# Kernel optimization log

Measured on AMD Instinct MI355X. Metric: run time of the kernel, lower is better.

Reference implementation:

```python
import jax, jax.numpy as jnp
import numpy as np

B, S, D, H = 2, 2048, 1024, 16
DH = D // H
EPS = 1e-5


def setup_inputs() -> dict:
    key = jax.random.key(0)
    ks = jax.random.split(key, 12)
    inp = {
        "Q_source": jax.random.normal(ks[0], (B, S, D), jnp.float32),
        "K_source": jax.random.normal(ks[1], (B, S, D), jnp.float32),
        "V_source": jax.random.normal(ks[2], (B, S, D), jnp.float32),
        "padding_mask": jnp.zeros((B, 1, 1, S), dtype=bool),  # no padded keys (avoids NaN rows)
        "future_mask": jnp.triu(jnp.ones((S, S), dtype=bool), k=1)[None, None],  # causal
    }
    sc = 1.0 / np.sqrt(D)
    names = ["WQ", "WK", "WV", "WO"]
    for i, n in enumerate(names):
        inp[n] = jax.random.normal(ks[3 + i], (D, D), jnp.float32) * sc
        inp["b" + n[1]] = jnp.zeros((D,), jnp.float32)
    inp["gamma"] = jnp.ones((D,), jnp.float32)
    inp["beta"] = jnp.zeros((D,), jnp.float32)
    return inp


def reference(Q_source, K_source, V_source, padding_mask, future_mask,
              WQ, bQ, WK, bK, WV, bV, WO, bO, gamma, beta):
    b = Q_source.shape[0]
    # torch Linear: x @ W.T + b ; reshape to [B, H, S, DH]
    def proj(x, W, bb):
        y = x @ W.T + bb
        return y.reshape(b, -1, H, DH).transpose(0, 2, 1, 3)

    Q = proj(Q_source, WQ, bQ)
    K = proj(K_source, WK, bK)
    V = proj(V_source, WV, bV)

    scores = jnp.einsum("bhqd,bhkd->bhqk", Q, K) / jnp.sqrt(jnp.float32(DH))
    neg_inf = jnp.float32(-jnp.inf)
    scores = jnp.where(padding_mask, neg_inf, scores)
    scores = jnp.where(future_mask, neg_inf, scores)
    attn = jax.nn.softmax(scores, axis=-1)

    ctx = jnp.einsum("bhqk,bhkd->bhqd", attn, V)
    ctx = ctx.transpose(0, 2, 1, 3).reshape(b, -1, D)
    out = ctx @ WO.T + bO

    x = Q_source + out
    mu = x.mean(-1, keepdims=True)
    var = x.var(-1, keepdims=True)
    return (x - mu) * jax.lax.rsqrt(var + EPS) * gamma + beta
```

## Files before the change

kernel.cpp:

```cpp
#include <hip/hip_runtime.h>

#define S_LEN 2048
#define DMODEL 1024
#define NH 16
#define DHD 64

typedef __attribute__((ext_vector_type(8))) short bh8;
typedef __attribute__((ext_vector_type(4))) float f32x4;
typedef __attribute__((ext_vector_type(2))) unsigned int u32x2;
typedef __attribute__((ext_vector_type(4))) unsigned int u32x4;
typedef unsigned short u16;
typedef unsigned int u32;

static __device__ __forceinline__ u16 f2bf(float f) {
    unsigned u = __builtin_bit_cast(unsigned, f);
    u += 0x7fffu + ((u >> 16) & 1u);
    return (u16)(u >> 16);
}

typedef const __attribute__((address_space(1))) void* gptr_t;
typedef __attribute__((address_space(3))) void* lptr_t;

static __device__ __forceinline__ void gll16(const void* g, void* l) {
    __builtin_amdgcn_global_load_lds((gptr_t)g, (lptr_t)l, 16, 0, 0);
}

__global__ __launch_bounds__(256) void cvt_all(const float* __restrict__ WQ, const float* __restrict__ WK,
                                               const float* __restrict__ WV, const float* __restrict__ WO,
                                               const float* __restrict__ S0, const float* __restrict__ S1,
                                               const float* __restrict__ S2,
                                               u16* __restrict__ wq, u16* __restrict__ wk,
                                               u16* __restrict__ wv, u16* __restrict__ wo,
                                               u16* __restrict__ q0, u16* __restrict__ k0,
                                               u16* __restrict__ v0) {
    int bid = blockIdx.x;
    const float* s;
    u16* o;
    size_t base;
    if (bid < 2048) {
        int wi = bid >> 9;
        s = wi == 0 ? WQ : (wi == 1 ? WK : (wi == 2 ? WV : WO));
        o = wi == 0 ? wq : (wi == 1 ? wk : (wi == 2 ? wv : wo));
        base = (size_t)(bid & 511) * 2048;
    } else {
        int r = bid - 2048;
        int si = r >> 11;
        s = si == 0 ? S0 : (si == 1 ? S1 : S2);
        o = si == 0 ? q0 : (si == 1 ? k0 : v0);
        base = (size_t)(r & 2047) * 2048;
    }
    size_t i = base + (size_t)threadIdx.x * 8;
    float4 a = *(const float4*)(s + i);
    float4 b = *(const float4*)(s + i + 4);
    u32 p0 = (u32)f2bf(a.x) | ((u32)f2bf(a.y) << 16);
    u32 p1 = (u32)f2bf(a.z) | ((u32)f2bf(a.w) << 16);
    u32 p2 = (u32)f2bf(b.x) | ((u32)f2bf(b.y) << 16);
    u32 p3 = (u32)f2bf(b.z) | ((u32)f2bf(b.w) << 16);
    *(u32x4*)(o + i) = (u32x4){p0, p1, p2, p3};
}

template <int BM, int OBF, int AF32>
static __device__ __forceinline__ void gemm_body(const void* __restrict__ Ap, const u16* __restrict__ Bm,
                                                 const float* __restrict__ bias, void* __restrict__ Cv,
                                                 int N, int K, int bi, int bj, short* Al, short* Bl,
                                                 float oscale) {
    constexpr int MI = BM / 32;
    constexpr int NC = BM / 64;
    int tid = threadIdx.x, lane = tid & 63, w = tid >> 6;
    int ln = lane & 15, hi = lane >> 4;
    int wm = w >> 1, wn = w & 1;
    f32x4 acc[MI][4];
#pragma unroll
    for (int i = 0; i < MI; i++)
#pragma unroll
        for (int j = 0; j < 4; j++) acc[i][j] = (f32x4){0.f, 0.f, 0.f, 0.f};
    int nk = K >> 5;

    float4 fa[NC][2];
    auto loadA = [&](int kt) {
#pragma unroll
        for (int c = 0; c < NC; ++c) {
            int o = c * 4096 + tid * 16;
            int row = o >> 6, e0 = (o & 63) >> 1;
            const float* src = (const float*)Ap + (size_t)(bi * BM + row) * K + kt * 32 + e0;
            fa[c][0] = *(const float4*)src;
            fa[c][1] = *(const float4*)(src + 4);
        }
    };
    auto writeA = [&](int buf) {
#pragma unroll
        for (int c = 0; c < NC; ++c) {
            int o = c * 4096 + tid * 16;
            u32 w0 = (u32)f2bf(fa[c][0].x) | ((u32)f2bf(fa[c][0].y) << 16);
            u32 w1 = (u32)f2bf(fa[c][0].z) | ((u32)f2bf(fa[c][0].w) << 16);
            u32 w2 = (u32)f2bf(fa[c][1].x) | ((u32)f2bf(fa[c][1].y) << 16);
            u32 w3 = (u32)f2bf(fa[c][1].z) | ((u32)f2bf(fa[c][1].w) << 16);
            *(u32x4*)((char*)(Al + buf * (BM * 32)) + o) = (u32x4){w0, w1, w2, w3};
        }
    };
    auto stageA_lds = [&](int buf, int kt) {
#pragma unroll
        for (int c = 0; c < NC; ++c) {
            int o = c * 4096 + tid * 16;
            int row = o >> 6, col = (o & 63) >> 1;
            gll16((const u16*)Ap + (size_t)(bi * BM + row) * K + kt * 32 + col,
                  (char*)(Al + buf * (BM * 32)) + o);
        }
    };
    auto stageB = [&](int buf, int kt) {
#pragma unroll
        for (int c = 0; c < 2; ++c) {
            int o = c * 4096 + tid * 16;
            int row = o >> 6, col = (o & 63) >> 1;
            gll16(Bm + (size_t)(bj * 128 + row) * K + kt * 32 + col, (char*)(Bl + buf * 4096) + o);
        }
    };

    if constexpr (AF32) { loadA(0); writeA(0); } else { stageA_lds(0, 0); }
    stageB(0, 0);
    __syncthreads();
    int cur = 0;
    for (int kt = 0; kt < nk; ++kt) {
        bool pre = (kt + 1 < nk);
        if (pre) {
            if constexpr (AF32) loadA(kt + 1); else stageA_lds(cur ^ 1, kt + 1);
            stageB(cur ^ 1, kt + 1);
        }
        bh8 av[MI], bv[4];
#pragma unroll
        for (int i = 0; i < MI; i++) av[i] = *(const bh8*)&Al[cur * (BM * 32) + (wm * (BM / 2) + i * 16 + ln) * 32 + hi * 8];
#pragma unroll
        for (int j = 0; j < 4; j++) bv[j] = *(const bh8*)&Bl[cur * 4096 + (wn * 64 + j * 16 + ln) * 32 + hi * 8];
#pragma unroll
        for (int i = 0; i < MI; i++)
#pragma unroll
            for (int j = 0; j < 4; j++)
                acc[i][j] = __builtin_amdgcn_mfma_f32_16x16x32_bf16(av[i], bv[j], acc[i][j], 0, 0, 0);
        if constexpr (AF32) { if (pre) writeA(cur ^ 1); }
        __syncthreads();
        cur ^= 1;
    }
    if constexpr (OBF == 2) {
#pragma unroll
        for (int j = 0; j < 4; j++) {
            int col = wn * 64 + j * 16 + ln;
            float bvs = bias[bj * 128 + col];
#pragma unroll
            for (int i = 0; i < MI; i++) {
                int row0 = wm * (BM / 2) + i * 16 + hi * 4;
                u32 p01 = (u32)f2bf(acc[i][j][0] + bvs) | ((u32)f2bf(acc[i][j][1] + bvs) << 16);
                u32 p23 = (u32)f2bf(acc[i][j][2] + bvs) | ((u32)f2bf(acc[i][j][3] + bvs) << 16);
                int idx = col * 128 + (row0 ^ ((col & 7) << 3));
                *(u32x2*)&Al[idx] = (u32x2){p01, p23};
            }
        }
        __syncthreads();
        int b = bi >> 4;
        int sbase = (bi & 15) * 128;
#pragma unroll
        for (int it = 0; it < 8; ++it) {
            int idx = it * 256 + tid;
            int dcol = idx >> 4;
            int sl = (idx & 15) * 8;
            bh8 v = *(const bh8*)&Al[dcol * 128 + (sl ^ ((dcol & 7) << 3))];
            int h = bj * 2 + (dcol >> 6), d = dcol & 63;
            *(bh8*)((u16*)Cv + ((size_t)((b * 16 + h) * 64 + d)) * 2048 + sbase + sl) = v;
        }
        return;
    }
#pragma unroll
    for (int j = 0; j < 4; j++) {
        int col = bj * 128 + wn * 64 + j * 16 + ln;
        float bvs = bias[col];
#pragma unroll
        for (int i = 0; i < MI; i++) {
            int row0 = bi * BM + wm * (BM / 2) + i * 16 + hi * 4;
#pragma unroll
            for (int rr = 0; rr < 4; rr++) {
                if (OBF) {
                    float v = (acc[i][j][rr] + bvs) * oscale;
                    ((u16*)Cv)[(size_t)(row0 + rr) * N + col] = f2bf(v);
                } else {
                    ((float*)Cv)[(size_t)(row0 + rr) * N + col] = acc[i][j][rr] + bvs;
                }
            }
        }
    }
}

__global__ __launch_bounds__(256, 3) void gemm_qkv(const u16* __restrict__ A0, const u16* __restrict__ A1,
                                                   const u16* __restrict__ A2, const u16* __restrict__ B0,
                                                   const u16* __restrict__ B1, const u16* __restrict__ B2,
                                                   const float* __restrict__ c0, const float* __restrict__ c1,
                                                   const float* __restrict__ c2, u16* __restrict__ C0,
                                                   u16* __restrict__ C1, u16* __restrict__ VT) {
    __shared__ short SH[16384];
    short* Al = SH;
    short* Bl = SH + 8192;
    int bid = blockIdx.x;
    int swz = (bid & 7) * 96 + (bid >> 3);
    int z = swz >> 8, t = swz & 255;
    if (z == 2) {
        gemm_body<128, 2, 0>(A2, B2, c2, VT, 1024, 1024, t >> 3, t & 7, Al, Bl, 1.0f);
    } else if (z == 0) {
        gemm_body<128, 1, 0>(A0, B0, c0, C0, 1024, 1024, t >> 3, t & 7, Al, Bl, 0.18033688f);
    } else {
        gemm_body<128, 1, 0>(A1, B1, c1, C1, 1024, 1024, t >> 3, t & 7, Al, Bl, 1.0f);
    }
}

__global__ __launch_bounds__(256) void gemm_o(const u16* __restrict__ A, const u16* __restrict__ Bm,
                                              const float* __restrict__ bias, float* __restrict__ C) {
    __shared__ short Al[2 * 64 * 32];
    __shared__ short Bl[2 * 128 * 32];
    int bid = blockIdx.x;
    int swz = (bid & 7) * 64 + (bid >> 3);
    gemm_body<64, 0, 0>(A, Bm, bias, C, 1024, 1024, swz >> 3, swz & 7, Al, Bl, 1.0f);
}

template <int PLO, int PHI>
static __device__ __forceinline__ void attn_core(const u16* __restrict__ Qp, const u16* __restrict__ Kp,
                                                 const u16* __restrict__ VT, u16* __restrict__ Ctx,
                                                 short* Klb, short* Vlb, short* Pw, float* Csh, float* Ls,
                                                 int b, int h, int bh, int qt, int tid) {
    int lane = tid & 63, w = tid >> 6;
    int grp = w >> 2;
    int qsub = w & 3;
    int tgl = tid & 255;
    int ln = lane & 15, hi = lane >> 4;
    __builtin_amdgcn_s_setprio(PLO);
    bh8 ones;
#pragma unroll
    for (int e = 0; e < 8; e++) ones[e] = (short)0x3F80;

    auto stage_kv = [&](int buf, int kt) {
#pragma unroll
        for (int c = 0; c < 2; ++c) {
            int o = c * 4096 + tgl * 16;
            int rr = o >> 7;
            int slot = (o >> 4) & 7;
            gll16(Kp + ((size_t)(b * S_LEN + kt * 64 + rr)) * DMODEL + h * DHD + ((slot ^ (rr & 7)) << 3),
                  (char*)(Klb + buf * 4096) + o);
            gll16(VT + ((size_t)(bh * DHD + rr)) * S_LEN + kt * 64 + ((slot ^ (rr & 7)) << 3),
                  (char*)(Vlb + buf * 4096) + o);
        }
    };

    int nh = qt + 1;
    int nt = 2 * qt + 2;
    int kbase = grp * nh;
    int qg0 = (qt << 7) + qsub * 32 + ln;
    const bh8* qr0 = (const bh8*)(Qp + ((size_t)(b * S_LEN + qg0)) * DMODEL + h * DHD);
    const bh8* qr1 = (const bh8*)(Qp + ((size_t)(b * S_LEN + qg0 + 16)) * DMODEL + h * DHD);
    bh8 qf[2][2];
    qf[0][0] = qr0[hi]; qf[0][1] = qr0[4 + hi];
    qf[1][0] = qr1[hi]; qf[1][1] = qr1[4 + hi];
    f32x4 ctxa[2][4];
    f32x4 lacc[2];
#pragma unroll
    for (int g = 0; g < 2; g++) {
        lacc[g] = (f32x4){0.f, 0.f, 0.f, 0.f};
#pragma unroll
        for (int i = 0; i < 4; i++) ctxa[g][i] = (f32x4){0.f, 0.f, 0.f, 0.f};
    }
    stage_kv(0, kbase);
    __syncthreads();
    int cur = 0;
    for (int i = 0; i < nh; ++i) {
        int kt = kbase + i;
        if (i + 1 < nh) stage_kv(cur ^ 1, kt + 1);
        f32x4 sc[2][4];
#pragma unroll
        for (int g = 0; g < 2; g++)
#pragma unroll
            for (int ks = 0; ks < 4; ++ks) sc[g][ks] = (f32x4){0.f, 0.f, 0.f, 0.f};
        __builtin_amdgcn_s_setprio(PHI);
#pragma unroll
        for (int dwin = 0; dwin < 2; ++dwin) {
#pragma unroll
            for (int ks = 0; ks < 4; ++ks) {
                int rr = ks * 16 + ln;
                bh8 kv = *(const bh8*)&Klb[cur * 4096 + rr * 64 + ((dwin * 32 + hi * 8) ^ ((rr & 7) << 3))];
                sc[0][ks] = __builtin_amdgcn_mfma_f32_16x16x32_bf16(kv, qf[0][dwin], sc[0][ks], 0, 0, 0);
                sc[1][ks] = __builtin_amdgcn_mfma_f32_16x16x32_bf16(kv, qf[1][dwin], sc[1][ks], 0, 0, 0);
            }
        }
        __builtin_amdgcn_s_setprio(PLO);
        if (kt >= nt - 2) {
#pragma unroll
            for (int g = 0; g < 2; g++) {
                int qgq = qg0 + g * 16;
#pragma unroll
                for (int ks = 0; ks < 4; ++ks)
#pragma unroll
                    for (int rr = 0; rr < 4; ++rr) {
                        int kg = kt * 64 + ks * 16 + hi * 4 + rr;
                        sc[g][ks][rr] = (kg <= qgq) ? sc[g][ks][rr] : -1e30f;
                    }
            }
        }
#pragma unroll
        for (int g = 0; g < 2; g++) {
#pragma unroll
            for (int ks = 0; ks < 4; ++ks) {
                u32 u0 = __builtin_bit_cast(u32, __builtin_amdgcn_exp2f(sc[g][ks][0]));
                u32 u1 = __builtin_bit_cast(u32, __builtin_amdgcn_exp2f(sc[g][ks][1]));
                u32 u2 = __builtin_bit_cast(u32, __builtin_amdgcn_exp2f(sc[g][ks][2]));
                u32 u3 = __builtin_bit_cast(u32, __builtin_amdgcn_exp2f(sc[g][ks][3]));
                u32 a01 = (u0 >> 16) | (u1 & 0xffff0000u);
                u32 a23 = (u2 >> 16) | (u3 & 0xffff0000u);
                int kloc = ks * 16 + hi * 4;
                *(u32x2*)&Pw[(g * 16 + ln) * 64 + (kloc ^ ((ln & 7) << 3))] = (u32x2){a01, a23};
            }
        }
        __builtin_amdgcn_s_setprio(PHI);
#pragma unroll
        for (int kw = 0; kw < 2; ++kw) {
            bh8 pf0 = *(const bh8*)&Pw[ln * 64 + ((kw * 32 + hi * 8) ^ ((ln & 7) << 3))];
            bh8 pf1 = *(const bh8*)&Pw[(16 + ln) * 64 + ((kw * 32 + hi * 8) ^ ((ln & 7) << 3))];
            lacc[0] = __builtin_amdgcn_mfma_f32_16x16x32_bf16(ones, pf0, lacc[0], 0, 0, 0);
            lacc[1] = __builtin_amdgcn_mfma_f32_16x16x32_bf16(ones, pf1, lacc[1], 0, 0, 0);
#pragma unroll
            for (int ds = 0; ds < 4; ++ds) {
                int d = ds * 16 + ln;
                bh8 vf = *(const bh8*)&Vlb[cur * 4096 + d * 64 + ((kw * 32 + hi * 8) ^ ((d & 7) << 3))];
                ctxa[0][ds] = __builtin_amdgcn_mfma_f32_16x16x32_bf16(vf, pf0, ctxa[0][ds], 0, 0, 0);
                ctxa[1][ds] = __builtin_amdgcn_mfma_f32_16x16x32_bf16(vf, pf1, ctxa[1][ds], 0, 0, 0);
            }
        }
        __builtin_amdgcn_s_setprio(PLO);
        __syncthreads();
        cur ^= 1;
    }
    __builtin_amdgcn_s_setprio(0);
    if (grp == 1) {
#pragma unroll
        for (int g = 0; g < 2; g++) {
            int qloc = g * 16 + ln;
#pragma unroll
            for (int ds = 0; ds < 4; ++ds) {
                int doff = (ds * 16 + hi * 4) ^ ((qloc & 7) << 3);
                *(f32x4*)&Csh[(qsub * 32 + qloc) * 64 + doff] = ctxa[g][ds];
            }
            if (hi == 0) Ls[qsub * 32 + qloc] = lacc[g][0];
        }
    }
    __syncthreads();
    if (grp == 0) {
#pragma unroll
        for (int g = 0; g < 2; g++) {
            int qloc = g * 16 + ln;
            float inv = 1.f / (lacc[g][0] + Ls[qsub * 32 + qloc]);
            u16* cp = Ctx + ((size_t)(b * S_LEN + qg0 + g * 16)) * DMODEL + h * DHD;
#pragma unroll
            for (int ds = 0; ds < 4; ++ds) {
                int doff = (ds * 16 + hi * 4) ^ ((qloc & 7) << 3);
                f32x4 p = *(const f32x4*)&Csh[(qsub * 32 + qloc) * 64 + doff];
                ushort4 st;
                st.x = f2bf((ctxa[g][ds][0] + p[0]) * inv);
                st.y = f2bf((ctxa[g][ds][1] + p[1]) * inv);
                st.z = f2bf((ctxa[g][ds][2] + p[2]) * inv);
                st.w = f2bf((ctxa[g][ds][3] + p[3]) * inv);
                *(ushort4*)(cp + ds * 16 + hi * 4) = st;
            }
        }
    }
}

__global__ __launch_bounds__(512, 1) void attn_fwd(const u16* __restrict__ Qp, const u16* __restrict__ Kp,
                                                   const u16* __restrict__ VT, u16* __restrict__ Ctx) {
    __shared__ short Kl[2][2][4096];
    __shared__ short Vl[2][2][4096];
    __shared__ short Pl[8][2048];
    __shared__ float Ls[128];
    int tid = threadIdx.x, w = tid >> 6;
    int grp = w >> 2;
    int bid = blockIdx.x;
    int rnd = bid >> 8, slot = bid & 255;
    int xcd = slot & 7, t = slot >> 3;
    int bh = xcd * 4 + (t & 3);
    int qte = t >> 2;
    int qt = rnd ? (15 - 2 * qte) : (2 * qte);
    int b = bh >> 4, h = bh & 15;
    float* Csh = (float*)&Kl[0][0][0];
    if (qt >= 8)
        attn_core<2, 3>(Qp, Kp, VT, Ctx, &Kl[grp][0][0], &Vl[grp][0][0], &Pl[w][0], Csh, Ls, b, h, bh, qt, tid);
    else
        attn_core<0, 1>(Qp, Kp, VT, Ctx, &Kl[grp][0][0], &Vl[grp][0][0], &Pl[w][0], Csh, Ls, b, h, bh, qt, tid);
}

__global__ __launch_bounds__(256) void ln_res(const float* __restrict__ Xres, const float* __restrict__ Y,
                                              const float* __restrict__ gamma, const float* __restrict__ beta,
                                              float* __restrict__ out) {
    int row = blockIdx.x, tid = threadIdx.x;
    const float4* xr = (const float4*)(Xres + (size_t)row * DMODEL);
    const float4* yr = (const float4*)(Y + (size_t)row * DMODEL);
    float4 a = xr[tid], bq = yr[tid];
    float x0 = a.x + bq.x, x1 = a.y + bq.y, x2 = a.z + bq.z, x3 = a.w + bq.w;
    float s1 = x0 + x1 + x2 + x3;
    float s2 = x0 * x0 + x1 * x1 + x2 * x2 + x3 * x3;
#pragma unroll
    for (int off = 32; off > 0; off >>= 1) {
        s1 += __shfl_xor(s1, off);
        s2 += __shfl_xor(s2, off);
    }
    __shared__ float r1[4], r2[4];
    int wv = tid >> 6;
    if ((tid & 63) == 0) { r1[wv] = s1; r2[wv] = s2; }
    __syncthreads();
    s1 = r1[0] + r1[1] + r1[2] + r1[3];
    s2 = r2[0] + r2[1] + r2[2] + r2[3];
    float mu = s1 * (1.0f / 1024.0f);
    float var = s2 * (1.0f / 1024.0f) - mu * mu;
    float rstd = rsqrtf(var + 1e-5f);
    const float4* g4 = (const float4*)gamma;
    const float4* b4 = (const float4*)beta;
    float4 g = g4[tid], bb = b4[tid];
    float4 res;
    res.x = (x0 - mu) * rstd * g.x + bb.x;
    res.y = (x1 - mu) * rstd * g.y + bb.y;
    res.z = (x2 - mu) * rstd * g.z + bb.z;
    res.w = (x3 - mu) * rstd * g.w + bb.w;
    *((float4*)(out + (size_t)row * DMODEL) + tid) = res;
}

extern "C" void kernel_launch(void* const* d_in, const int* in_sizes, int n_in,
                              void* d_out, int out_size, void* d_ws, size_t ws_size,
                              hipStream_t stream) {
    const float* Qs = (const float*)d_in[0];
    const float* Ks = (const float*)d_in[1];
    const float* Vs = (const float*)d_in[2];
    const float* WQ = (const float*)d_in[5];
    const float* bQ = (const float*)d_in[6];
    const float* WK = (const float*)d_in[7];
    const float* bK = (const float*)d_in[8];
    const float* WV = (const float*)d_in[9];
    const float* bV = (const float*)d_in[10];
    const float* WO = (const float*)d_in[11];
    const float* bO = (const float*)d_in[12];
    const float* gamma = (const float*)d_in[13];
    const float* beta = (const float*)d_in[14];

    const size_t MB = 1u << 20;
    char* w8 = (char*)d_ws;
    u16* Qb  = (u16*)(w8 + 0 * MB);
    u16* Kb  = (u16*)(w8 + 8 * MB);
    u16* Vb  = (u16*)(w8 + 16 * MB);
    u16* WQb = (u16*)(w8 + 24 * MB);
    u16* WKb = (u16*)(w8 + 26 * MB);
    u16* WVb = (u16*)(w8 + 28 * MB);
    u16* WOb = (u16*)(w8 + 30 * MB);
    u16* Qp  = (u16*)(w8 + 32 * MB);
    u16* Kp  = (u16*)(w8 + 40 * MB);
    u16* VTb = (u16*)(w8 + 56 * MB);
    u16* Ctx = (u16*)(w8 + 64 * MB);
    float* Y2 = (float*)(w8 + 72 * MB);

    cvt_all<<<8192, 256, 0, stream>>>(WQ, WK, WV, WO, Qs, Ks, Vs, WQb, WKb, WVb, WOb, Qb, Kb, Vb);
    gemm_qkv<<<768, 256, 0, stream>>>(Qb, Kb, Vb, WQb, WKb, WVb, bQ, bK, bV, Qp, Kp, VTb);
    attn_fwd<<<512, 512, 0, stream>>>(Qp, Kp, VTb, Ctx);
    gemm_o<<<512, 256, 0, stream>>>(Ctx, WOb, bO, Y2);
    ln_res<<<4096, 256, 0, stream>>>(Qs, Y2, gamma, beta, (float*)d_out);
}
```

Before: 112.9 us.

## Replace MFMA rowsum with scalar sums, halve P scratch, raise attention occupancy

The softmax denominator is now accumulated as fp32 scalar sums with cross-lane shuffles, replacing the extra MFMA against a vector of ones. The P tile is written and consumed one 16-row group at a time, which halves the per-wave P scratch, and the row-sum buffer now aliases a P buffer. Launch bounds go from 1 to 4 blocks per CU, and the block mapping changes from a zigzag over two rounds to descending query tiles so the longest causal tiles start first. The tighter register budget may cause spills, and processing the groups one after the other adds LDS round trips and reduces MFMA interleaving.

Result: slower. 117.9 us (+4.4%).

```diff
diff --git a/kernel.cpp b/kernel.cpp
--- a/kernel.cpp
+++ b/kernel.cpp
@@ -221,7 +221,7 @@
 template <int PLO, int PHI>
 static __device__ __forceinline__ void attn_core(const u16* __restrict__ Qp, const u16* __restrict__ Kp,
                                                  const u16* __restrict__ VT, u16* __restrict__ Ctx,
-                                                 short* Klb, short* Vlb, short* Pw, float* Csh, float* Ls,
+                                                 short* Klb, short* Vlb, short* Pw, float* Csh, float* Lsh,
                                                  int b, int h, int bh, int qt, int tid) {
     int lane = tid & 63, w = tid >> 6;
     int grp = w >> 2;
@@ -229,9 +229,6 @@
     int tgl = tid & 255;
     int ln = lane & 15, hi = lane >> 4;
     __builtin_amdgcn_s_setprio(PLO);
-    bh8 ones;
-#pragma unroll
-    for (int e = 0; e < 8; e++) ones[e] = (short)0x3F80;
 
     auto stage_kv = [&](int buf, int kt) {
 #pragma unroll
@@ -256,13 +253,11 @@
     qf[0][0] = qr0[hi]; qf[0][1] = qr0[4 + hi];
     qf[1][0] = qr1[hi]; qf[1][1] = qr1[4 + hi];
     f32x4 ctxa[2][4];
-    f32x4 lacc[2];
-#pragma unroll
-    for (int g = 0; g < 2; g++) {
-        lacc[g] = (f32x4){0.f, 0.f, 0.f, 0.f};
+    float ls[2] = {0.f, 0.f};
+#pragma unroll
+    for (int g = 0; g < 2; g++)
 #pragma unroll
         for (int i = 0; i < 4; i++) ctxa[g][i] = (f32x4){0.f, 0.f, 0.f, 0.f};
-    }
     stage_kv(0, kbase);
     __syncthreads();
     int cur = 0;
@@ -303,34 +298,40 @@
         for (int g = 0; g < 2; g++) {
 #pragma unroll
             for (int ks = 0; ks < 4; ++ks) {
-                u32 u0 = __builtin_bit_cast(u32, __builtin_amdgcn_exp2f(sc[g][ks][0]));
-                u32 u1 = __builtin_bit_cast(u32, __builtin_amdgcn_exp2f(sc[g][ks][1]));
-                u32 u2 = __builtin_bit_cast(u32, __builtin_amdgcn_exp2f(sc[g][ks][2]));
-                u32 u3 = __builtin_bit_cast(u32, __builtin_amdgcn_exp2f(sc[g][ks][3]));
+                float p0 = __builtin_amdgcn_exp2f(sc[g][ks][0]);
+                float p1 = __builtin_amdgcn_exp2f(sc[g][ks][1]);
+                float p2 = __builtin_amdgcn_exp2f(sc[g][ks][2]);
+                float p3 = __builtin_amdgcn_exp2f(sc[g][ks][3]);
+                ls[g] += (p0 + p1) + (p2 + p3);
+                u32 u0 = __builtin_bit_cast(u32, p0);
+                u32 u1 = __builtin_bit_cast(u32, p1);
+                u32 u2 = __builtin_bit_cast(u32, p2);
+                u32 u3 = __builtin_bit_cast(u32, p3);
                 u32 a01 = (u0 >> 16) | (u1 & 0xffff0000u);
                 u32 a23 = (u2 >> 16) | (u3 & 0xffff0000u);
                 int kloc = ks * 16 + hi * 4;
-                *(u32x2*)&Pw[(g * 16 + ln) * 64 + (kloc ^ ((ln & 7) << 3))] = (u32x2){a01, a23};
-            }
-        }
-        __builtin_amdgcn_s_setprio(PHI);
-#pragma unroll
-        for (int kw = 0; kw < 2; ++kw) {
-            bh8 pf0 = *(const bh8*)&Pw[ln * 64 + ((kw * 32 + hi * 8) ^ ((ln & 7) << 3))];
-            bh8 pf1 = *(const bh8*)&Pw[(16 + ln) * 64 + ((kw * 32 + hi * 8) ^ ((ln & 7) << 3))];
-            lacc[0] = __builtin_amdgcn_mfma_f32_16x16x32_bf16(ones, pf0, lacc[0], 0, 0, 0);
-            lacc[1] = __builtin_amdgcn_mfma_f32_16x16x32_bf16(ones, pf1, lacc[1], 0, 0, 0);
-#pragma unroll
-            for (int ds = 0; ds < 4; ++ds) {
-                int d = ds * 16 + ln;
-                bh8 vf = *(const bh8*)&Vlb[cur * 4096 + d * 64 + ((kw * 32 + hi * 8) ^ ((d & 7) << 3))];
-                ctxa[0][ds] = __builtin_amdgcn_mfma_f32_16x16x32_bf16(vf, pf0, ctxa[0][ds], 0, 0, 0);
-                ctxa[1][ds] = __builtin_amdgcn_mfma_f32_16x16x32_bf16(vf, pf1, ctxa[1][ds], 0, 0, 0);
-            }
-        }
-        __builtin_amdgcn_s_setprio(PLO);
+                *(u32x2*)&Pw[ln * 64 + (kloc ^ ((ln & 7) << 3))] = (u32x2){a01, a23};
+            }
+            __builtin_amdgcn_s_setprio(PHI);
+#pragma unroll
+            for (int kw = 0; kw < 2; ++kw) {
+                bh8 pf = *(const bh8*)&Pw[ln * 64 + ((kw * 32 + hi * 8) ^ ((ln & 7) << 3))];
+#pragma unroll
+                for (int ds = 0; ds < 4; ++ds) {
+                    int d = ds * 16 + ln;
+                    bh8 vf = *(const bh8*)&Vlb[cur * 4096 + d * 64 + ((kw * 32 + hi * 8) ^ ((d & 7) << 3))];
+                    ctxa[g][ds] = __builtin_amdgcn_mfma_f32_16x16x32_bf16(vf, pf, ctxa[g][ds], 0, 0, 0);
+                }
+            }
+            __builtin_amdgcn_s_setprio(PLO);
+        }
         __syncthreads();
         cur ^= 1;
+    }
+#pragma unroll
+    for (int g = 0; g < 2; g++) {
+        ls[g] += __shfl_xor(ls[g], 16);
+        ls[g] += __shfl_xor(ls[g], 32);
     }
     __builtin_amdgcn_s_setprio(0);
     if (grp == 1) {
@@ -342,7 +343,7 @@
                 int doff = (ds * 16 + hi * 4) ^ ((qloc & 7) << 3);
                 *(f32x4*)&Csh[(qsub * 32 + qloc) * 64 + doff] = ctxa[g][ds];
             }
-            if (hi == 0) Ls[qsub * 32 + qloc] = lacc[g][0];
+            if (hi == 0) Lsh[qsub * 32 + qloc] = ls[g];
         }
     }
     __syncthreads();
@@ -350,7 +351,7 @@
 #pragma unroll
         for (int g = 0; g < 2; g++) {
             int qloc = g * 16 + ln;
-            float inv = 1.f / (lacc[g][0] + Ls[qsub * 32 + qloc]);
+            float inv = 1.f / (ls[g] + Lsh[qsub * 32 + qloc]);
             u16* cp = Ctx + ((size_t)(b * S_LEN + qg0 + g * 16)) * DMODEL + h * DHD;
 #pragma unroll
             for (int ds = 0; ds < 4; ++ds) {
@@ -367,26 +368,24 @@
     }
 }
 
-__global__ __launch_bounds__(512, 1) void attn_fwd(const u16* __restrict__ Qp, const u16* __restrict__ Kp,
+__global__ __launch_bounds__(512, 4) void attn_fwd(const u16* __restrict__ Qp, const u16* __restrict__ Kp,
                                                    const u16* __restrict__ VT, u16* __restrict__ Ctx) {
     __shared__ short Kl[2][2][4096];
     __shared__ short Vl[2][2][4096];
-    __shared__ short Pl[8][2048];
-    __shared__ float Ls[128];
+    __shared__ short Pl[8][1024];
     int tid = threadIdx.x, w = tid >> 6;
     int grp = w >> 2;
     int bid = blockIdx.x;
-    int rnd = bid >> 8, slot = bid & 255;
-    int xcd = slot & 7, t = slot >> 3;
-    int bh = xcd * 4 + (t & 3);
-    int qte = t >> 2;
-    int qt = rnd ? (15 - 2 * qte) : (2 * qte);
+    int xcd = bid & 7;
+    int qt = 15 - (bid >> 5);
+    int bh = xcd * 4 + ((bid >> 3) & 3);
     int b = bh >> 4, h = bh & 15;
     float* Csh = (float*)&Kl[0][0][0];
+    float* Lsh = (float*)&Pl[4][0];
     if (qt >= 8)
-        attn_core<2, 3>(Qp, Kp, VT, Ctx, &Kl[grp][0][0], &Vl[grp][0][0], &Pl[w][0], Csh, Ls, b, h, bh, qt, tid);
+        attn_core<2, 3>(Qp, Kp, VT, Ctx, &Kl[grp][0][0], &Vl[grp][0][0], &Pl[w][0], Csh, Lsh, b, h, bh, qt, tid);
     else
-        attn_core<0, 1>(Qp, Kp, VT, Ctx, &Kl[grp][0][0], &Vl[grp][0][0], &Pl[w][0], Csh, Ls, b, h, bh, qt, tid);
+        attn_core<0, 1>(Qp, Kp, VT, Ctx, &Kl[grp][0][0], &Vl[grp][0][0], &Pl[w][0], Csh, Lsh, b, h, bh, qt, tid);
 }
 
 __global__ __launch_bounds__(256) void ln_res(const float* __restrict__ Xres, const float* __restrict__ Y,
```
